# Kernel optimization log

Hardware: AMD Instinct MI355X
Metric: run time of the kernel (lower is better)

Reference implementation:

```python
import jax, jax.numpy as jnp
import numpy as np

D_MODEL = 1024
N_HEADS = 16
D_HEAD = D_MODEL // N_HEADS
LN_EPS = 1e-5


def setup_inputs() -> dict:
    key = jax.random.key(0)
    ks = jax.random.split(key, 10)
    B, N = 2, 2048
    s = 1.0 / np.sqrt(D_MODEL)
    return {
        "x": jax.random.normal(ks[0], (B, N, D_MODEL), dtype=jnp.float32),
        "Wq": jax.random.normal(ks[1], (D_MODEL, D_MODEL), dtype=jnp.float32) * s,
        "bq": jnp.zeros((D_MODEL,), dtype=jnp.float32),
        "Wk": jax.random.normal(ks[2], (D_MODEL, D_MODEL), dtype=jnp.float32) * s,
        "bk": jnp.zeros((D_MODEL,), dtype=jnp.float32),
        "Wv": jax.random.normal(ks[3], (D_MODEL, D_MODEL), dtype=jnp.float32) * s,
        "bv": jnp.zeros((D_MODEL,), dtype=jnp.float32),
        "Wo": jax.random.normal(ks[4], (D_MODEL, D_MODEL), dtype=jnp.float32) * s,
        "bo": jnp.zeros((D_MODEL,), dtype=jnp.float32),
        "ln_gamma": jnp.ones((D_MODEL,), dtype=jnp.float32),
        "ln_beta": jnp.zeros((D_MODEL,), dtype=jnp.float32),
    }


def reference(x, Wq, bq, Wk, bk, Wv, bv, Wo, bo, ln_gamma, ln_beta):
    B, N, _ = x.shape
    # QKV projections -> [B, H, N, dh]
    def proj(W, b):
        return (x @ W.T + b).reshape(B, N, N_HEADS, D_HEAD).transpose(0, 2, 1, 3)
    Q, K, V = proj(Wq, bq), proj(Wk, bk), proj(Wv, bv)
    # scaled scores [B, H, N, N] with causal mask (is_mask=True)
    scores = jnp.einsum("bhqd,bhkd->bhqk", Q, K) / np.sqrt(D_HEAD)
    causal = jnp.tril(jnp.ones((N, N), dtype=bool))
    scores = jnp.where(causal, scores, -jnp.inf)
    attn = jax.nn.softmax(scores, axis=-1)  # dropout p=0 (eval)
    ctx = jnp.einsum("bhqk,bhkd->bhqd", attn, V)  # [B, H, N, dh]
    ctx = ctx.transpose(0, 2, 1, 3).reshape(B, N, D_MODEL)
    out = ctx @ Wo.T + bo + x  # output proj + residual
    # LayerNorm over last dim
    mu = out.mean(-1, keepdims=True)
    var = out.var(-1, keepdims=True)
    return (out - mu) / jnp.sqrt(var + LN_EPS) * ln_gamma + ln_beta
```

## Files before the change

### kernel.cpp

```cpp
#include <hip/hip_runtime.h>
#include <type_traits>

#define D_MODEL 1024
#define NHEADS 16
#define DHEAD 64
#define SEQ 2048
#define BATCH 2
#define MROWS (BATCH*SEQ)
#define NQT (SEQ/64)

typedef unsigned short ushort_t;
typedef unsigned int   u32;
using bf16x8 = __attribute__((ext_vector_type(8))) __bf16;
using bf16x4 = __attribute__((ext_vector_type(4))) __bf16;
using us4    = __attribute__((ext_vector_type(4))) unsigned short;
using us8    = __attribute__((ext_vector_type(8))) unsigned short;
using f32x4  = __attribute__((ext_vector_type(4))) float;
using f32x2  = __attribute__((ext_vector_type(2))) float;

#define QSCALE 0.18033688011112042f

__device__ __forceinline__ float fast_exp2(float x) {
#if __has_builtin(__builtin_amdgcn_exp2f)
    return __builtin_amdgcn_exp2f(x);
#else
    return __expf(x * 0.6931471805599453f);
#endif
}

__device__ __forceinline__ void gl2lds(const ushort_t* g, ushort_t* l) {
    __builtin_amdgcn_global_load_lds(
        (const __attribute__((address_space(1))) unsigned int*)g,
        (__attribute__((address_space(3))) unsigned int*)l,
        16, 0, 0);
}

__global__ __launch_bounds__(256) void cvt_kernel(
    const float* __restrict__ x,
    const float* __restrict__ wq, const float* __restrict__ wk,
    const float* __restrict__ wv, const float* __restrict__ wo,
    ushort_t* __restrict__ xb,
    ushort_t* __restrict__ wqb, ushort_t* __restrict__ wkb,
    ushort_t* __restrict__ wvb, ushort_t* __restrict__ wob)
{
    const size_t XN = (size_t)MROWS * D_MODEL;
    const size_t WN = (size_t)D_MODEL * D_MODEL;
    size_t i = ((size_t)blockIdx.x * 256 + threadIdx.x) * 4;
    const float* s; ushort_t* d; size_t off;
    if (i < XN) { s = x; d = xb; off = i; }
    else {
        size_t j = i - XN;
        int w = (int)(j / WN);
        off = j - (size_t)w * WN;
        s = (w == 0) ? wq : (w == 1) ? wk : (w == 2) ? wv : wo;
        d = (w == 0) ? wqb : (w == 1) ? wkb : (w == 2) ? wvb : wob;
    }
    const f32x4 v = *(const f32x4*)(s + off);
    bf16x4 o;
    #pragma unroll
    for (int t = 0; t < 4; ++t) o[t] = (__bf16)v[t];
    *(bf16x4*)(d + off) = o;
}

template<typename OutT, bool RES, bool M64>
__global__ __launch_bounds__(256, 3) void gemm_nt(
    const ushort_t* __restrict__ A,
    const ushort_t* __restrict__ W0, const ushort_t* __restrict__ W1, const ushort_t* __restrict__ W2,
    const float* __restrict__ b0, const float* __restrict__ b1, const float* __restrict__ b2,
    const float* __restrict__ res,
    OutT* __restrict__ Y0, OutT* __restrict__ Y1, OutT* __restrict__ Y2,
    float qsc)
{
    constexpr int K = D_MODEL;
    constexpr int BM = M64 ? 64 : 128;
    constexpr int MR = M64 ? 2 : 4;
    __shared__ ushort_t As[2][BM * 32];
    __shared__ ushort_t Ws[2][128 * 32];

    const int z = blockIdx.z;
    const ushort_t* W  = (z == 0) ? W0 : (z == 1) ? W1 : W2;
    const float* bias  = (z == 0) ? b0 : (z == 1) ? b1 : b2;
    OutT* Y            = (z == 0) ? Y0 : (z == 1) ? Y1 : Y2;
    const float sc     = (z == 0) ? qsc : 1.0f;

    const int i0 = blockIdx.x * BM;
    const int j0 = blockIdx.y * 128;
    const int tid  = threadIdx.x;
    const int lane = tid & 63;
    const int w    = tid >> 6;
    const int wm   = (w >> 1) * (M64 ? 32 : 64);
    const int wn   = (w & 1) * 64;
    const int l15  = lane & 15;
    const int quad = lane >> 4;

    const int srow = lane >> 2;
    const int scol = ((lane & 3) ^ ((lane >> 3) & 3)) * 8;
    const int ca0 = M64 ? w : (w * 2);
    const int ca1 = w * 2 + 1;
    const int c0 = w * 2, c1 = w * 2 + 1;
    const ushort_t* gA0 = A + (size_t)(i0 + ca0 * 16 + srow) * K + scol;
    const ushort_t* gA1 = A + (size_t)(i0 + ca1 * 16 + srow) * K + scol;
    const ushort_t* gW0 = W + (size_t)(j0 + c0 * 16 + srow) * K + scol;
    const ushort_t* gW1 = W + (size_t)(j0 + c1 * 16 + srow) * K + scol;

    const int rc = (quad ^ ((l15 >> 1) & 3)) * 8;

    f32x4 acc[MR][4] = {};

    for (int k0 = 0; k0 < K; k0 += 64) {
        gl2lds(gA0 + k0,      &As[0][ca0 * 512]);
        if constexpr (!M64) gl2lds(gA1 + k0, &As[0][ca1 * 512]);
        gl2lds(gA0 + k0 + 32, &As[1][ca0 * 512]);
        if constexpr (!M64) gl2lds(gA1 + k0 + 32, &As[1][ca1 * 512]);
        gl2lds(gW0 + k0,      &Ws[0][c0 * 512]);
        gl2lds(gW1 + k0,      &Ws[0][c1 * 512]);
        gl2lds(gW0 + k0 + 32, &Ws[1][c0 * 512]);
        gl2lds(gW1 + k0 + 32, &Ws[1][c1 * 512]);
        __syncthreads();

        #pragma unroll
        for (int s = 0; s < 2; ++s) {
            bf16x8 af[MR], wf[4];
            #pragma unroll
            for (int m = 0; m < MR; ++m)
                af[m] = *(const bf16x8*)&As[s][(wm + m * 16 + l15) * 32 + rc];
            #pragma unroll
            for (int n = 0; n < 4; ++n)
                wf[n] = *(const bf16x8*)&Ws[s][(wn + n * 16 + l15) * 32 + rc];
            #pragma unroll
            for (int m = 0; m < MR; ++m)
                #pragma unroll
                for (int n = 0; n < 4; ++n)
                    acc[m][n] = __builtin_amdgcn_mfma_f32_16x16x32_bf16(wf[n], af[m], acc[m][n], 0, 0, 0);
        }
        __syncthreads();
    }

    #pragma unroll
    for (int n = 0; n < 4; ++n) {
        const int col = j0 + wn + n * 16 + quad * 4;
        const f32x4 bv = *(const f32x4*)&bias[col];
        #pragma unroll
        for (int m = 0; m < MR; ++m) {
            const int row = i0 + wm + m * 16 + l15;
            if constexpr (std::is_same<OutT, float>::value) {
                f32x4 v;
                #pragma unroll
                for (int r = 0; r < 4; ++r) v[r] = acc[m][n][r] + bv[r];
                if constexpr (RES) {
                    const f32x4 rv = *(const f32x4*)&res[(size_t)row * D_MODEL + col];
                    #pragma unroll
                    for (int r = 0; r < 4; ++r) v[r] += rv[r];
                }
                *(f32x4*)&Y[(size_t)row * D_MODEL + col] = v;
            } else {
                bf16x4 pk;
                #pragma unroll
                for (int r = 0; r < 4; ++r) pk[r] = (__bf16)((acc[m][n][r] + bv[r]) * sc);
                *(bf16x4*)&Y[(size_t)row * D_MODEL + col] = pk;
            }
        }
    }
}

#define KD 64

__global__ __launch_bounds__(256, 3) void attn_kernel(
    const ushort_t* __restrict__ Qg, const ushort_t* __restrict__ Kg,
    const ushort_t* __restrict__ Vg, ushort_t* __restrict__ Og,
    float* __restrict__ wso, float* __restrict__ wsml)
{
    __shared__ __align__(16) ushort_t Kt[2][64 * KD];
    __shared__ __align__(16) ushort_t Vt[2][64 * KD];
    __shared__ __align__(16) ushort_t Pw[128 * KD];

    const int bh = blockIdx.x;
    const int b = bh >> 4;
    const int h = bh & 15;

    const int y = blockIdx.y;
    int qp, kt0, kt1, part;
    bool heavy;
    if (y < 16) {
        const int t = y & 7;
        qp = 15 - t;
        part = y >> 3;
        const int nkt = 2 * qp + 2;
        const int hh = qp + 1;
        heavy = true;
        if (part) { kt0 = hh; kt1 = nkt; }
        else      { kt0 = 0;  kt1 = hh;  }
    } else {
        qp = y - 16;
        part = 0;
        kt0 = 0; kt1 = 2 * qp + 2;
        heavy = false;
    }
    const int qtL = 2 * qp;
    const int qtU = 2 * qp + 1;
    const int q0 = qp * 128;

    const int tid  = threadIdx.x;
    const int lane = tid & 63;
    const int w    = tid >> 6;
    const int l15  = lane & 15;
    const int quad = lane >> 4;

    const size_t headoff = (size_t)h * DHEAD;
    const ushort_t* Kbase = Kg + (size_t)(b * SEQ) * D_MODEL + headoff;
    const ushort_t* Vbase = Vg + (size_t)(b * SEQ) * D_MODEL + headoff;

    const int krow = tid >> 3;
    const int kb   = tid & 7;
    const int vkey = tid & 63;
    const int dc0  = tid >> 6;
    const int dc1  = dc0 + 4;

    const int rx = (l15 & 7) << 3;
    const int cs0 = (quad * 8) ^ rx;
    const int cs1 = (32 + quad * 8) ^ rx;
    int pwc[4];
    #pragma unroll
    for (int f = 0; f < 4; ++f) pwc[f] = (f * 16 + quad * 4) ^ rx;
    ushort_t* PwRowL = &Pw[(w * 16 + l15) * KD];
    ushort_t* PwRowU = &Pw[(64 + w * 16 + l15) * KD];

    const int kwa = krow * KD + ((kb * 8) ^ ((krow & 7) << 3));

    const int qgL = q0 + w * 16 + l15;
    const int qgU = q0 + 64 + w * 16 + l15;
    const size_t qrowL = (size_t)(b * SEQ + qgL) * D_MODEL + headoff;
    const size_t qrowU = (size_t)(b * SEQ + qgU) * D_MODEL + headoff;
    const bf16x8 qf0L = *(const bf16x8*)&Qg[qrowL + quad * 8];
    const bf16x8 qf1L = *(const bf16x8*)&Qg[qrowL + 32 + quad * 8];
    const bf16x8 qf0U = *(const bf16x8*)&Qg[qrowU + quad * 8];
    const bf16x8 qf1U = *(const bf16x8*)&Qg[qrowU + 32 + quad * 8];

    bf16x8 onesf;
    #pragma unroll
    for (int j = 0; j < 8; ++j) onesf[j] = (__bf16)1.0f;

    float m_runL = -1e30f, m_runU = -1e30f;
    f32x4 oL[4] = {}, oU[4] = {};
    f32x4 o4L = {}, o4U = {};

    us8 kp0, kp1, vp0, vp1;
    const size_t koff0 = (size_t)(kt0 * 64) * D_MODEL;
    kp0 = *(const us8*)&Kbase[koff0 + (size_t)krow * D_MODEL + kb * 8];
    kp1 = *(const us8*)&Kbase[koff0 + (size_t)(32 + krow) * D_MODEL + kb * 8];
    vp0 = *(const us8*)&Vbase[koff0 + (size_t)vkey * D_MODEL + dc0 * 8];
    vp1 = *(const us8*)&Vbase[koff0 + (size_t)vkey * D_MODEL + dc1 * 8];
    *(us8*)&Kt[0][kwa]           = kp0;
    *(us8*)&Kt[0][kwa + 32 * KD] = kp1;
    #pragma unroll
    for (int j = 0; j < 8; ++j) {
        Vt[0][(dc0 * 8 + j) * KD + (vkey ^ (j << 3))] = vp0[j];
        Vt[0][(dc1 * 8 + j) * KD + (vkey ^ (j << 3))] = vp1[j];
    }
    __syncthreads();

    for (int kt = kt0; kt < kt1; ++kt) {
        const int cur = (kt - kt0) & 1;
        const int nxt = cur ^ 1;
        const bool pre = (kt + 1 < kt1);
        const bool actL = (kt <= qtL);
        if (pre) {
            const size_t koff = (size_t)((kt + 1) * 64) * D_MODEL;
            kp0 = *(const us8*)&Kbase[koff + (size_t)krow * D_MODEL + kb * 8];
            kp1 = *(const us8*)&Kbase[koff + (size_t)(32 + krow) * D_MODEL + kb * 8];
            vp0 = *(const us8*)&Vbase[koff + (size_t)vkey * D_MODEL + dc0 * 8];
            vp1 = *(const us8*)&Vbase[koff + (size_t)vkey * D_MODEL + dc1 * 8];
        }

        f32x4 svL[4], svU[4];
        __builtin_amdgcn_s_setprio(1);
        #pragma unroll
        for (int f = 0; f < 4; ++f) {
            const int rbase = (f * 16 + l15) * KD;
            const bf16x8 kf0 = *(const bf16x8*)&Kt[cur][rbase + cs0];
            const bf16x8 kf1 = *(const bf16x8*)&Kt[cur][rbase + cs1];
            f32x4 sU = {};
            sU = __builtin_amdgcn_mfma_f32_16x16x32_bf16(kf0, qf0U, sU, 0, 0, 0);
            sU = __builtin_amdgcn_mfma_f32_16x16x32_bf16(kf1, qf1U, sU, 0, 0, 0);
            svU[f] = sU;
            f32x4 sL = {};
            sL = __builtin_amdgcn_mfma_f32_16x16x32_bf16(kf0, qf0L, sL, 0, 0, 0);
            sL = __builtin_amdgcn_mfma_f32_16x16x32_bf16(kf1, qf1L, sL, 0, 0, 0);
            svL[f] = sL;
        }
        __builtin_amdgcn_s_setprio(0);

        if (kt == qtU) {
            #pragma unroll
            for (int f = 0; f < 4; ++f)
                #pragma unroll
                for (int r = 0; r < 4; ++r) {
                    const int kg = kt * 64 + f * 16 + quad * 4 + r;
                    svU[f][r] = (kg <= qgU) ? svU[f][r] : -1e30f;
                }
        }
        if (kt == qtL) {
            #pragma unroll
            for (int f = 0; f < 4; ++f)
                #pragma unroll
                for (int r = 0; r < 4; ++r) {
                    const int kg = kt * 64 + f * 16 + quad * 4 + r;
                    svL[f][r] = (kg <= qgL) ? svL[f][r] : -1e30f;
                }
        }

        {
            float mf[4];
            #pragma unroll
            for (int f = 0; f < 4; ++f)
                mf[f] = fmaxf(fmaxf(svU[f][0], svU[f][1]), fmaxf(svU[f][2], svU[f][3]));
            float mx = fmaxf(fmaxf(mf[0], mf[1]), fmaxf(mf[2], mf[3]));
            mx = fmaxf(mx, __shfl_xor(mx, 16));
            mx = fmaxf(mx, __shfl_xor(mx, 32));
            if (!__all(mx <= m_runU + 8.0f)) {
                const float mn = fmaxf(m_runU, mx);
                const float al = fast_exp2(m_runU - mn);
                m_runU = mn;
                #pragma unroll
                for (int t = 0; t < 4; ++t)
                    #pragma unroll
                    for (int r = 0; r < 4; ++r) oU[t][r] *= al;
                o4U[0] *= al;
            }
            #pragma unroll
            for (int f = 0; f < 4; ++f) {
                bf16x4 pk;
                #pragma unroll
                for (int r = 0; r < 4; ++r)
                    pk[r] = (__bf16)fast_exp2(svU[f][r] - m_runU);
                *(bf16x4*)&PwRowU[pwc[f]] = pk;
            }
        }
        if (actL) {
            float mf[4];
            #pragma unroll
            for (int f = 0; f < 4; ++f)
                mf[f] = fmaxf(fmaxf(svL[f][0], svL[f][1]), fmaxf(svL[f][2], svL[f][3]));
            float mx = fmaxf(fmaxf(mf[0], mf[1]), fmaxf(mf[2], mf[3]));
            mx = fmaxf(mx, __shfl_xor(mx, 16));
            mx = fmaxf(mx, __shfl_xor(mx, 32));
            if (!__all(mx <= m_runL + 8.0f)) {
                const float mn = fmaxf(m_runL, mx);
                const float al = fast_exp2(m_runL - mn);
                m_runL = mn;
                #pragma unroll
                for (int t = 0; t < 4; ++t)
                    #pragma unroll
                    for (int r = 0; r < 4; ++r) oL[t][r] *= al;
                o4L[0] *= al;
            }
            #pragma unroll
            for (int f = 0; f < 4; ++f) {
                bf16x4 pk;
                #pragma unroll
                for (int r = 0; r < 4; ++r)
                    pk[r] = (__bf16)fast_exp2(svL[f][r] - m_runL);
                *(bf16x4*)&PwRowL[pwc[f]] = pk;
            }
        }
        __asm__ volatile("s_waitcnt lgkmcnt(0)" ::: "memory");

        __builtin_amdgcn_s_setprio(1);
        #pragma unroll
        for (int s = 0; s < 2; ++s) {
            const int cc = s ? cs1 : cs0;
            const bf16x8 pfU = *(const bf16x8*)&PwRowU[cc];
            if (actL) {
                const bf16x8 pfL = *(const bf16x8*)&PwRowL[cc];
                #pragma unroll
                for (int t = 0; t < 4; ++t) {
                    const bf16x8 vf = *(const bf16x8*)&Vt[cur][(t * 16 + l15) * KD + cc];
                    oU[t] = __builtin_amdgcn_mfma_f32_16x16x32_bf16(vf, pfU, oU[t], 0, 0, 0);
                    oL[t] = __builtin_amdgcn_mfma_f32_16x16x32_bf16(vf, pfL, oL[t], 0, 0, 0);
                }
                o4U = __builtin_amdgcn_mfma_f32_16x16x32_bf16(onesf, pfU, o4U, 0, 0, 0);
                o4L = __builtin_amdgcn_mfma_f32_16x16x32_bf16(onesf, pfL, o4L, 0, 0, 0);
            } else {
                #pragma unroll
                for (int t = 0; t < 4; ++t) {
                    const bf16x8 vf = *(const bf16x8*)&Vt[cur][(t * 16 + l15) * KD + cc];
                    oU[t] = __builtin_amdgcn_mfma_f32_16x16x32_bf16(vf, pfU, oU[t], 0, 0, 0);
                }
                o4U = __builtin_amdgcn_mfma_f32_16x16x32_bf16(onesf, pfU, o4U, 0, 0, 0);
            }
        }
        __builtin_amdgcn_s_setprio(0);

        if (pre) {
            *(us8*)&Kt[nxt][kwa]           = kp0;
            *(us8*)&Kt[nxt][kwa + 32 * KD] = kp1;
            #pragma unroll
            for (int j = 0; j < 8; ++j) {
                Vt[nxt][(dc0 * 8 + j) * KD + (vkey ^ (j << 3))] = vp0[j];
                Vt[nxt][(dc1 * 8 + j) * KD + (vkey ^ (j << 3))] = vp1[j];
            }
        }
        __asm__ volatile("s_waitcnt lgkmcnt(0)\n\ts_barrier" ::: "memory");
    }

    if (!heavy) {
        const float invL = 1.f / o4L[0];
        const float invU = 1.f / o4U[0];
        const size_t orowL = (size_t)(b * SEQ + qgL) * D_MODEL + headoff;
        const size_t orowU = (size_t)(b * SEQ + qgU) * D_MODEL + headoff;
        #pragma unroll
        for (int t = 0; t < 4; ++t) {
            bf16x4 pkL, pkU;
            #pragma unroll
            for (int r = 0; r < 4; ++r) {
                pkL[r] = (__bf16)(oL[t][r] * invL);
                pkU[r] = (__bf16)(oU[t][r] * invU);
            }
            *(bf16x4*)&Og[orowL + t * 16 + quad * 4] = pkL;
            *(bf16x4*)&Og[orowU + t * 16 + quad * 4] = pkU;
        }
    } else {
        const int T = (bh * 8 + (qp - 8)) * 2 + part;
        const int rL = w * 16 + l15;
        const int rU = 64 + w * 16 + l15;
        float* wo = wso + (size_t)T * 8192;
        #pragma unroll
        for (int t = 0; t < 4; ++t) {
            *(f32x4*)&wo[(size_t)rL * 64 + t * 16 + quad * 4] = oL[t];
            *(f32x4*)&wo[(size_t)rU * 64 + t * 16 + quad * 4] = oU[t];
        }
        if (quad == 0) {
            f32x2 mlL = { m_runL, o4L[0] };
            f32x2 mlU = { m_runU, o4U[0] };
            *(f32x2*)&wsml[(size_t)(T * 128 + rL) * 2] = mlL;
            *(f32x2*)&wsml[(size_t)(T * 128 + rU) * 2] = mlU;
        }
    }
}

__global__ __launch_bounds__(256) void attn_combine(
    const float* __restrict__ wso, const float* __restrict__ wsml,
    ushort_t* __restrict__ Og)
{
    const int gid = blockIdx.x * 256 + threadIdx.x;
    const int row = gid >> 4;
    const int dp  = (gid & 15) * 4;
    const int bh  = row >> 10;
    const int rr  = row & 1023;
    const int qph = rr >> 7;
    const int q   = rr & 127;
    const int T0  = (bh * 8 + qph) * 2;

    const f32x2 ml0 = *(const f32x2*)&wsml[(size_t)(T0 * 128 + q) * 2];
    const f32x2 ml1 = *(const f32x2*)&wsml[(size_t)((T0 + 1) * 128 + q) * 2];
    const float M  = fmaxf(ml0[0], ml1[0]);
    const float a0 = fast_exp2(ml0[0] - M);
    const float a1 = fast_exp2(ml1[0] - M);
    const float inv = 1.0f / (ml0[1] * a0 + ml1[1] * a1);

    const f32x4 o0 = *(const f32x4*)&wso[(size_t)T0 * 8192 + q * 64 + dp];
    const f32x4 o1 = *(const f32x4*)&wso[(size_t)(T0 + 1) * 8192 + q * 64 + dp];

    const int b = bh >> 4;
    const int h = bh & 15;
    const int qg = 1024 + rr;
    bf16x4 pk;
    #pragma unroll
    for (int r = 0; r < 4; ++r)
        pk[r] = (__bf16)((o0[r] * a0 + o1[r] * a1) * inv);
    *(bf16x4*)&Og[(size_t)(b * SEQ + qg) * D_MODEL + h * DHEAD + dp] = pk;
}

__global__ __launch_bounds__(256) void ln_kernel(
    const float* __restrict__ X, const float* __restrict__ g,
    const float* __restrict__ bta, float* __restrict__ out)
{
    __shared__ float r1[4], r2[4];
    const int row = blockIdx.x;
    const int tid = threadIdx.x;
    const float* p = X + (size_t)row * D_MODEL;
    float v[4]; float s1 = 0.f, s2 = 0.f;
    #pragma unroll
    for (int i = 0; i < 4; ++i) { v[i] = p[tid + 256 * i]; s1 += v[i]; s2 += v[i] * v[i]; }
    #pragma unroll
    for (int d = 32; d >= 1; d >>= 1) { s1 += __shfl_xor(s1, d); s2 += __shfl_xor(s2, d); }
    if ((tid & 63) == 0) { r1[tid >> 6] = s1; r2[tid >> 6] = s2; }
    __syncthreads();
    s1 = r1[0] + r1[1] + r1[2] + r1[3];
    s2 = r2[0] + r2[1] + r2[2] + r2[3];
    const float mu  = s1 * (1.f / D_MODEL);
    const float var = s2 * (1.f / D_MODEL) - mu * mu;
    const float rstd = rsqrtf(var + 1e-5f);
    #pragma unroll
    for (int i = 0; i < 4; ++i) {
        const int c = tid + 256 * i;
        out[(size_t)row * D_MODEL + c] = (v[i] - mu) * rstd * g[c] + bta[c];
    }
}

extern "C" void kernel_launch(void* const* d_in, const int* in_sizes, int n_in,
                              void* d_out, int out_size, void* d_ws, size_t ws_size,
                              hipStream_t stream) {
    const float* x     = (const float*)d_in[0];
    const float* Wq    = (const float*)d_in[1];
    const float* bq    = (const float*)d_in[2];
    const float* Wk    = (const float*)d_in[3];
    const float* bk    = (const float*)d_in[4];
    const float* Wv    = (const float*)d_in[5];
    const float* bv    = (const float*)d_in[6];
    const float* Wo    = (const float*)d_in[7];
    const float* bo    = (const float*)d_in[8];
    const float* gamma = (const float*)d_in[9];
    const float* beta  = (const float*)d_in[10];

    const size_t XN = (size_t)MROWS * D_MODEL;
    const size_t WN = (size_t)D_MODEL * D_MODEL;
    ushort_t* wsp = (ushort_t*)d_ws;
    ushort_t* xb  = wsp;
    ushort_t* Yq  = wsp + XN;
    ushort_t* Yk  = wsp + 2 * XN;
    ushort_t* Yv  = wsp + 3 * XN;
    ushort_t* Wqb = wsp + 4 * XN;
    ushort_t* Wkb = Wqb + WN;
    ushort_t* Wvb = Wkb + WN;
    ushort_t* Wob = Wvb + WN;
    ushort_t* ctx = xb;
    float*    pre = (float*)d_out;

    float* wso  = (float*)(wsp + 4 * XN + 4 * WN);
    float* wsml = wso + (size_t)512 * 8192;

    cvt_kernel<<<dim3(8192), 256, 0, stream>>>(x, Wq, Wk, Wv, Wo, xb, Wqb, Wkb, Wvb, Wob);

    gemm_nt<ushort_t, false, false><<<dim3(MROWS / 128, D_MODEL / 128, 3), 256, 0, stream>>>(
        xb, Wqb, Wkb, Wvb, bq, bk, bv, nullptr, Yq, Yk, Yv, QSCALE);

    attn_kernel<<<dim3(BATCH * NHEADS, 24), 256, 0, stream>>>(Yq, Yk, Yv, ctx, wso, wsml);

    attn_combine<<<dim3(2048), 256, 0, stream>>>(wso, wsml, ctx);

    gemm_nt<float, true, true><<<dim3(MROWS / 64, D_MODEL / 128, 1), 256, 0, stream>>>(
        ctx, Wob, Wob, Wob, bo, bo, bo, x, pre, pre, pre, 1.0f);

    ln_kernel<<<dim3(MROWS), 256, 0, stream>>>(pre, gamma, beta, (float*)d_out);
}
```

Before: 197.2 us.

## Fuse split-KV attention combine into attention kernel via last-block atomic counter

Removes the separate attn_combine launch. Each heavy attention block writes its partial output and softmax statistics, then increments a per-pair atomic counter. The second block to finish reads its partner's partial, merges the two, and writes the bf16 context directly. Counters are zeroed in the conversion kernel. This saves a kernel launch and half of the workspace re-reads, at the cost of extra fences and barriers in the heavy blocks.

```diff
diff --git a/kernel.cpp b/kernel.cpp
--- a/kernel.cpp
+++ b/kernel.cpp
@@ -41,8 +41,10 @@
     const float* __restrict__ wv, const float* __restrict__ wo,
     ushort_t* __restrict__ xb,
     ushort_t* __restrict__ wqb, ushort_t* __restrict__ wkb,
-    ushort_t* __restrict__ wvb, ushort_t* __restrict__ wob)
+    ushort_t* __restrict__ wvb, ushort_t* __restrict__ wob,
+    u32* __restrict__ wcnt)
 {
+    if (blockIdx.x == 0 && threadIdx.x < 256) wcnt[threadIdx.x] = 0;
     const size_t XN = (size_t)MROWS * D_MODEL;
     const size_t WN = (size_t)D_MODEL * D_MODEL;
     size_t i = ((size_t)blockIdx.x * 256 + threadIdx.x) * 4;
@@ -168,11 +170,12 @@
 __global__ __launch_bounds__(256, 3) void attn_kernel(
     const ushort_t* __restrict__ Qg, const ushort_t* __restrict__ Kg,
     const ushort_t* __restrict__ Vg, ushort_t* __restrict__ Og,
-    float* __restrict__ wso, float* __restrict__ wsml)
+    float* __restrict__ wso, float* __restrict__ wsml, u32* __restrict__ wcnt)
 {
     __shared__ __align__(16) ushort_t Kt[2][64 * KD];
     __shared__ __align__(16) ushort_t Vt[2][64 * KD];
     __shared__ __align__(16) ushort_t Pw[128 * KD];
+    __shared__ int s_last;
 
     const int bh = blockIdx.x;
     const int b = bh >> 4;
@@ -420,9 +423,11 @@
             *(bf16x4*)&Og[orowU + t * 16 + quad * 4] = pkU;
         }
     } else {
-        const int T = (bh * 8 + (qp - 8)) * 2 + part;
+        const int pairIdx = bh * 8 + (qp - 8);
+        const int T  = pairIdx * 2 + part;
+        const int Tp = T ^ 1;
         const int rL = w * 16 + l15;
-        const int rU = 64 + w * 16 + l15;
+        const int rU = 64 + rL;
         float* wo = wso + (size_t)T * 8192;
         #pragma unroll
         for (int t = 0; t < 4; ++t) {
@@ -435,40 +440,40 @@
             *(f32x2*)&wsml[(size_t)(T * 128 + rL) * 2] = mlL;
             *(f32x2*)&wsml[(size_t)(T * 128 + rU) * 2] = mlU;
         }
-    }
-}
-
-__global__ __launch_bounds__(256) void attn_combine(
-    const float* __restrict__ wso, const float* __restrict__ wsml,
-    ushort_t* __restrict__ Og)
-{
-    const int gid = blockIdx.x * 256 + threadIdx.x;
-    const int row = gid >> 4;
-    const int dp  = (gid & 15) * 4;
-    const int bh  = row >> 10;
-    const int rr  = row & 1023;
-    const int qph = rr >> 7;
-    const int q   = rr & 127;
-    const int T0  = (bh * 8 + qph) * 2;
-
-    const f32x2 ml0 = *(const f32x2*)&wsml[(size_t)(T0 * 128 + q) * 2];
-    const f32x2 ml1 = *(const f32x2*)&wsml[(size_t)((T0 + 1) * 128 + q) * 2];
-    const float M  = fmaxf(ml0[0], ml1[0]);
-    const float a0 = fast_exp2(ml0[0] - M);
-    const float a1 = fast_exp2(ml1[0] - M);
-    const float inv = 1.0f / (ml0[1] * a0 + ml1[1] * a1);
-
-    const f32x4 o0 = *(const f32x4*)&wso[(size_t)T0 * 8192 + q * 64 + dp];
-    const f32x4 o1 = *(const f32x4*)&wso[(size_t)(T0 + 1) * 8192 + q * 64 + dp];
-
-    const int b = bh >> 4;
-    const int h = bh & 15;
-    const int qg = 1024 + rr;
-    bf16x4 pk;
-    #pragma unroll
-    for (int r = 0; r < 4; ++r)
-        pk[r] = (__bf16)((o0[r] * a0 + o1[r] * a1) * inv);
-    *(bf16x4*)&Og[(size_t)(b * SEQ + qg) * D_MODEL + h * DHEAD + dp] = pk;
+        __threadfence();
+        __syncthreads();
+        if (tid == 0) s_last = (int)atomicAdd(&wcnt[pairIdx], 1u);
+        __syncthreads();
+        if (s_last == 1) {
+            __threadfence();
+            const float* po = wso + (size_t)Tp * 8192;
+            const f32x2 mpL = *(const f32x2*)&wsml[(size_t)(Tp * 128 + rL) * 2];
+            const f32x2 mpU = *(const f32x2*)&wsml[(size_t)(Tp * 128 + rU) * 2];
+            const float ML  = fmaxf(m_runL, mpL[0]);
+            const float aoL = fast_exp2(m_runL - ML);
+            const float apL = fast_exp2(mpL[0] - ML);
+            const float ivL = 1.0f / (o4L[0] * aoL + mpL[1] * apL);
+            const float MU  = fmaxf(m_runU, mpU[0]);
+            const float aoU = fast_exp2(m_runU - MU);
+            const float apU = fast_exp2(mpU[0] - MU);
+            const float ivU = 1.0f / (o4U[0] * aoU + mpU[1] * apU);
+            const size_t orowL = (size_t)(b * SEQ + qgL) * D_MODEL + headoff;
+            const size_t orowU = (size_t)(b * SEQ + qgU) * D_MODEL + headoff;
+            #pragma unroll
+            for (int t = 0; t < 4; ++t) {
+                const f32x4 pL = *(const f32x4*)&po[(size_t)rL * 64 + t * 16 + quad * 4];
+                const f32x4 pU = *(const f32x4*)&po[(size_t)rU * 64 + t * 16 + quad * 4];
+                bf16x4 kL, kU;
+                #pragma unroll
+                for (int r = 0; r < 4; ++r) {
+                    kL[r] = (__bf16)((oL[t][r] * aoL + pL[r] * apL) * ivL);
+                    kU[r] = (__bf16)((oU[t][r] * aoU + pU[r] * apU) * ivU);
+                }
+                *(bf16x4*)&Og[orowL + t * 16 + quad * 4] = kL;
+                *(bf16x4*)&Og[orowU + t * 16 + quad * 4] = kU;
+            }
+        }
+    }
 }
 
 __global__ __launch_bounds__(256) void ln_kernel(
@@ -529,15 +534,14 @@
 
     float* wso  = (float*)(wsp + 4 * XN + 4 * WN);
     float* wsml = wso + (size_t)512 * 8192;
-
-    cvt_kernel<<<dim3(8192), 256, 0, stream>>>(x, Wq, Wk, Wv, Wo, xb, Wqb, Wkb, Wvb, Wob);
+    u32*   wcnt = (u32*)(wsml + (size_t)512 * 128 * 2);
+
+    cvt_kernel<<<dim3(8192), 256, 0, stream>>>(x, Wq, Wk, Wv, Wo, xb, Wqb, Wkb, Wvb, Wob, wcnt);
 
     gemm_nt<ushort_t, false, false><<<dim3(MROWS / 128, D_MODEL / 128, 3), 256, 0, stream>>>(
         xb, Wqb, Wkb, Wvb, bq, bk, bv, nullptr, Yq, Yk, Yv, QSCALE);
 
-    attn_kernel<<<dim3(BATCH * NHEADS, 24), 256, 0, stream>>>(Yq, Yk, Yv, ctx, wso, wsml);
-
-    attn_combine<<<dim3(2048), 256, 0, stream>>>(wso, wsml, ctx);
+    attn_kernel<<<dim3(BATCH * NHEADS, 24), 256, 0, stream>>>(Yq, Yk, Yv, ctx, wso, wsml, wcnt);
 
     gemm_nt<float, true, true><<<dim3(MROWS / 64, D_MODEL / 128, 1), 256, 0, stream>>>(
         ctx, Wob, Wob, Wob, bo, bo, bo, x, pre, pre, pre, 1.0f);
```

Result: slower. 289.3 us (+46.7%).
